# Kernel optimization log

Hardware: AMD Instinct MI355X
Metric: run time of the kernel (lower is better)

## Reference

```python
import jax, jax.numpy as jnp
import numpy as np

NUM_HEADS = 12
D_MODEL = 768
D_HEAD = D_MODEL // NUM_HEADS


def setup_inputs() -> dict:
    key = jax.random.key(0)
    k_x, k_wqkv, k_bqkv, k_wo, k_bo = jax.random.split(key, 5)
    B, S = 1, 4096
    x = jax.random.normal(k_x, (B, S, D_MODEL), dtype=jnp.float32)
    # flax Dense default init: lecun_normal for kernel, zeros for bias
    w_qkv = jax.random.normal(k_wqkv, (D_MODEL, 3 * D_MODEL), dtype=jnp.float32) / np.sqrt(D_MODEL)
    b_qkv = jnp.zeros((3 * D_MODEL,), dtype=jnp.float32)
    w_o = jax.random.normal(k_wo, (D_MODEL, D_MODEL), dtype=jnp.float32) / np.sqrt(D_MODEL)
    b_o = jnp.zeros((D_MODEL,), dtype=jnp.float32)
    return {"x": x, "w_qkv": w_qkv, "b_qkv": b_qkv, "w_o": w_o, "b_o": b_o}


def reference(x, w_qkv, b_qkv, w_o, b_o):
    B, S, _ = x.shape
    H, Dh = NUM_HEADS, D_HEAD
    qkv = jnp.einsum('bsd,de->bse', x, w_qkv) + b_qkv  # [B,S,3*D]
    q, k, v = jnp.split(qkv, 3, axis=-1)
    # [B,S,D] -> [B,H,S,Dh]
    q = q.reshape(B, S, H, Dh).transpose(0, 2, 1, 3)
    k = k.reshape(B, S, H, Dh).transpose(0, 2, 1, 3)
    v = v.reshape(B, S, H, Dh).transpose(0, 2, 1, 3)
    logits = jnp.einsum('bhqd,bhkd->bhqk', q, k) / jnp.sqrt(jnp.float32(Dh))
    weights = jax.nn.softmax(logits, axis=-1)  # deterministic=True -> no dropout
    attn = jnp.einsum('bhqk,bhkd->bhqd', weights, v)
    attn = attn.transpose(0, 2, 1, 3).reshape(B, S, H * Dh)
    return jnp.einsum('bsd,de->bse', attn, w_o) + b_o
```

## Files before the change

kernel.cpp:

```cpp
#include <hip/hip_runtime.h>

typedef unsigned short u16;
typedef __attribute__((ext_vector_type(8))) short bf16x8;
typedef __attribute__((ext_vector_type(4))) float f32x4;

#define CST 0.18033688011112042f

__device__ inline u16 f2bf(float f) {
    unsigned u;
    __builtin_memcpy(&u, &f, 4);
    unsigned r = (u + 0x7FFF + ((u >> 16) & 1)) >> 16;
    return (u16)r;
}
__device__ inline unsigned pack2(float lo, float hi) {
    return (unsigned)f2bf(lo) | ((unsigned)f2bf(hi) << 16);
}
__device__ inline unsigned fbits(float f) {
    unsigned u;
    __builtin_memcpy(&u, &f, 4);
    return u;
}
__device__ inline f32x4 fzero() {
    f32x4 z = {0.f, 0.f, 0.f, 0.f};
    return z;
}
__device__ inline f32x4 mfma16(bf16x8 a, bf16x8 b, f32x4 c) {
    return __builtin_amdgcn_mfma_f32_16x16x32_bf16(a, b, c, 0, 0, 0);
}

__device__ inline void gld_lds16(const u16* g, u16* l) {
    __builtin_amdgcn_global_load_lds(
        reinterpret_cast<const __attribute__((address_space(1))) unsigned int*>(
            reinterpret_cast<uintptr_t>(g)),
        reinterpret_cast<__attribute__((address_space(3))) unsigned int*>(
            static_cast<unsigned int>(reinterpret_cast<uintptr_t>(l))),
        16, 0, 0);
}

#define NB_WQKV (72 * 24)
#define NB_WO   (24 * 24)
#define NB_CVT  (4096 * 768 / 2048)

__global__ __launch_bounds__(256) void prep(const float* __restrict__ x,
                                            const float* __restrict__ w_qkv,
                                            const float* __restrict__ w_o,
                                            u16* __restrict__ xb,
                                            u16* __restrict__ wqkvT,
                                            u16* __restrict__ woT) {
    __shared__ float tile[32][33];
    int bid = blockIdx.x;
    int t = threadIdx.x;
    if (bid < NB_WQKV + NB_WO) {
        const float* in;
        u16* out;
        int bx, by, R, C;
        if (bid < NB_WQKV) {
            in = w_qkv; out = wqkvT; R = 768; C = 2304;
            bx = bid % 72; by = bid / 72;
        } else {
            int b2 = bid - NB_WQKV;
            in = w_o; out = woT; R = 768; C = 768;
            bx = b2 % 24; by = b2 / 24;
        }
        int c0 = bx * 32, r0 = by * 32;
        int tx = t & 31, ty = t >> 5;
#pragma unroll
        for (int j = 0; j < 32; j += 8)
            tile[ty + j][tx] = in[(size_t)(r0 + ty + j) * C + c0 + tx];
        __syncthreads();
#pragma unroll
        for (int j = 0; j < 32; j += 8)
            out[(size_t)(c0 + ty + j) * R + r0 + tx] = f2bf(tile[tx][ty + j]);
    } else {
        int i = (bid - NB_WQKV - NB_WO) * 2048 + t * 8;
        float4 a = *(const float4*)(x + i);
        float4 b = *(const float4*)(x + i + 4);
        uint4 w;
        w.x = pack2(a.x, a.y);
        w.y = pack2(a.z, a.w);
        w.z = pack2(b.x, b.y);
        w.w = pack2(b.z, b.w);
        *(uint4*)(xb + i) = w;
    }
}

__global__ __launch_bounds__(256) void vtrans(const u16* __restrict__ qkv,
                                              u16* __restrict__ vt) {
    __shared__ u16 T[64 * 136];
    int t = threadIdx.x;
    int h = blockIdx.y, kv0 = blockIdx.x * 128;
    {
        int key = t >> 1, ch = (t & 1) * 32;
        const u16* vp = qkv + (size_t)(kv0 + key) * 2304 + 1536 + h * 64 + ch;
        u16 tmp[32];
        *(uint4*)&tmp[0]  = *(const uint4*)vp;
        *(uint4*)&tmp[8]  = *(const uint4*)(vp + 8);
        *(uint4*)&tmp[16] = *(const uint4*)(vp + 16);
        *(uint4*)&tmp[24] = *(const uint4*)(vp + 24);
        int k5 = key & 31, grp = key >> 5;
        int kp = (grp << 5) | (((k5 >> 2) & 3) << 3) | ((k5 >> 4) << 2) | (k5 & 3);
#pragma unroll
        for (int j = 0; j < 32; j++) T[(ch + j) * 136 + kp] = tmp[j];
    }
    __syncthreads();
    {
        int dh = t >> 2, kc = (t & 3) * 32;
        uint4 o0 = *(const uint4*)&T[dh * 136 + kc];
        uint4 o1 = *(const uint4*)&T[dh * 136 + kc + 8];
        uint4 o2 = *(const uint4*)&T[dh * 136 + kc + 16];
        uint4 o3 = *(const uint4*)&T[dh * 136 + kc + 24];
        u16* op = vt + ((size_t)(h * 64 + dh)) * 4096 + kv0 + kc;
        *(uint4*)op = o0;
        *(uint4*)(op + 8) = o1;
        *(uint4*)(op + 16) = o2;
        *(uint4*)(op + 24) = o3;
    }
}

template <int MT, bool OUT_F32, bool SCALE_Q>
__global__ __launch_bounds__(256) void gemm_bt(const u16* __restrict__ A,
                                               const u16* __restrict__ Bt,
                                               const float* __restrict__ bias,
                                               void* __restrict__ Cv,
                                               int M, int N, int K) {
    constexpr int MI = MT / 32;
    constexpr int NA = MT / 64;
    constexpr int AH = MT * 32;
    constexpr int BH = 128 * 32;
    __shared__ u16 As[2 * AH];
    __shared__ u16 Bs[2 * BH];

    int t = threadIdx.x;
    int wave = t >> 6, lane = t & 63, quad = lane >> 4, l16 = lane & 15;
    int mbase = blockIdx.y * MT, nbase = blockIdx.x * 128;
    int mw = (wave & 1) * (MT / 2), nw = (wave >> 1) * 64;

    f32x4 acc[MI][4];
#pragma unroll
    for (int i = 0; i < MI; i++)
#pragma unroll
        for (int j = 0; j < 4; j++) acc[i][j] = fzero();

    int xqs = (lane & 3) ^ ((lane >> 3) & 3);
    const u16* AgL[NA];
    u16* AsL[NA];
#pragma unroll
    for (int j = 0; j < NA; j++) {
        int rl = wave * (MT / 4) + j * 16 + (lane >> 2);
        AgL[j] = A + (size_t)(mbase + rl) * K + xqs * 8;
        AsL[j] = As + wave * (MT / 4) * 32 + j * 512;
    }
    const u16* BgL[2];
    u16* BsL[2];
#pragma unroll
    for (int j = 0; j < 2; j++) {
        int rl = wave * 32 + j * 16 + (lane >> 2);
        BgL[j] = Bt + (size_t)(nbase + rl) * K + xqs * 8;
        BsL[j] = Bs + wave * 1024 + j * 512;
    }

    auto STAGE = [&](int buf, int kt) {
#pragma unroll
        for (int j = 0; j < NA; j++) gld_lds16(AgL[j] + kt, AsL[j] + buf * AH);
#pragma unroll
        for (int j = 0; j < 2; j++) gld_lds16(BgL[j] + kt, BsL[j] + buf * BH);
    };

    int xq = quad ^ ((l16 >> 1) & 3);
    int afo[MI], bfo[4];
#pragma unroll
    for (int i = 0; i < MI; i++) afo[i] = (mw + i * 16 + l16) * 32 + xq * 8;
#pragma unroll
    for (int i = 0; i < 4; i++) bfo[i] = (nw + i * 16 + l16) * 32 + xq * 8;

    STAGE(0, 0);
    __syncthreads();

    int cur = 0;
    for (int kt = 0; kt < K; kt += 32) {
        if (kt + 32 < K) STAGE(cur ^ 1, kt + 32);

        const u16* AsB = As + cur * AH;
        const u16* BsB = Bs + cur * BH;
        bf16x8 af[MI], bfr[4];
#pragma unroll
        for (int i = 0; i < MI; i++) af[i] = *(const bf16x8*)&AsB[afo[i]];
#pragma unroll
        for (int i = 0; i < 4; i++) bfr[i] = *(const bf16x8*)&BsB[bfo[i]];
#pragma unroll
        for (int mi = 0; mi < MI; mi++)
#pragma unroll
            for (int ni = 0; ni < 4; ni++)
                acc[mi][ni] = mfma16(af[mi], bfr[ni], acc[mi][ni]);

        __syncthreads();
        cur ^= 1;
    }

#pragma unroll
    for (int ni = 0; ni < 4; ni++) {
        int col = nbase + nw + ni * 16 + l16;
        float bv = bias[col];
        float scale = (SCALE_Q && col < 768) ? CST : 1.0f;
#pragma unroll
        for (int mi = 0; mi < MI; mi++) {
#pragma unroll
            for (int r = 0; r < 4; r++) {
                int row = mbase + mw + mi * 16 + quad * 4 + r;
                float v = (acc[mi][ni][r] + bv) * scale;
                if (OUT_F32)
                    ((float*)Cv)[(size_t)row * N + col] = v;
                else
                    ((u16*)Cv)[(size_t)row * N + col] = f2bf(v);
            }
        }
    }
}

#define SEQ 4096
#define QKV_LD 2304

__global__ __launch_bounds__(256, 4) void attn_flash(const u16* __restrict__ qkv,
                                                     const u16* __restrict__ vt,
                                                     u16* __restrict__ attn) {
    __shared__ __align__(16) char smem[32768];

    int t = threadIdx.x;
    int wave = t >> 6, lane = t & 63, quad = lane >> 4, l16 = lane & 15;
    int kw = wave & 1, qw = wave >> 1;
    int h = blockIdx.y;
    int q0 = blockIdx.x * 64;
    const int QOFF = h * 64, KOFF = 768 + h * 64;

    bf16x8 qf[2][2];
#pragma unroll
    for (int qs = 0; qs < 2; qs++) {
        const u16* qp = qkv + (size_t)(q0 + qw * 32 + qs * 16 + l16) * QKV_LD + QOFF + quad * 8;
        qf[qs][0] = *(const bf16x8*)(qp);
        qf[qs][1] = *(const bf16x8*)(qp + 32);
    }

    f32x4 o[2][4];
    float l4[2];
#pragma unroll
    for (int qs = 0; qs < 2; qs++) {
        l4[qs] = 0.f;
#pragma unroll
        for (int j = 0; j < 4; j++) o[qs][j] = fzero();
    }

    const u16* kgl[2];
    int kofs[2];
#pragma unroll
    for (int j = 0; j < 2; j++) {
        int r = wave * 16 + j * 8 + (lane >> 3);
        kgl[j] = qkv + (size_t)r * QKV_LD + KOFF +
                 (((lane & 7) ^ ((lane >> 3) & 7)) * 8);
        kofs[j] = (wave * 16 + j * 8) * 64;
    }
    const u16* vgl[2];
    int vofs[2];
#pragma unroll
    for (int j = 0; j < 2; j++) {
        int r = wave * 16 + j * 8 + (lane >> 3);
        vgl[j] = vt + (size_t)(h * 64 + r) * SEQ +
                 (((lane & 7) ^ ((lane >> 3) & 7)) * 8);
        vofs[j] = (wave * 16 + j * 8) * 64;
    }

    auto STAGE = [&](int buf, int kv) {
        u16* kb = (u16*)(smem + buf * 8192);
        u16* vb = (u16*)(smem + 16384 + buf * 8192);
#pragma unroll
        for (int j = 0; j < 2; j++) gld_lds16(kgl[j] + (size_t)kv * QKV_LD, kb + kofs[j]);
#pragma unroll
        for (int j = 0; j < 2; j++) gld_lds16(vgl[j] + kv, vb + vofs[j]);
    };

    STAGE(0, 0);
    __syncthreads();

    int cur = 0;
    int x7 = l16 & 7;
    for (int kv0 = 0; kv0 < SEQ; kv0 += 64) {
        if (kv0 + 64 < SEQ) STAGE(cur ^ 1, kv0 + 64);

        const u16* KsB = (const u16*)(smem + cur * 8192);
        const u16* VsB = (const u16*)(smem + 16384 + cur * 8192);

        bf16x8 kf[2][2];
#pragma unroll
        for (int st = 0; st < 2; st++) {
            int r = kw * 32 + st * 16 + l16;
            kf[st][0] = *(const bf16x8*)&KsB[r * 64 + (quad ^ x7) * 8];
            kf[st][1] = *(const bf16x8*)&KsB[r * 64 + ((quad + 4) ^ x7) * 8];
        }
        bf16x8 vf[4];
#pragma unroll
        for (int nt = 0; nt < 4; nt++) {
            int r = nt * 16 + l16;
            vf[nt] = *(const bf16x8*)&VsB[r * 64 + ((kw * 4 + quad) ^ x7) * 8];
        }

        __builtin_amdgcn_s_setprio(1);
#pragma unroll
        for (int qs = 0; qs < 2; qs++) {
            f32x4 s0 = mfma16(kf[0][0], qf[qs][0], fzero());
            s0 = mfma16(kf[0][1], qf[qs][1], s0);
            f32x4 s1 = mfma16(kf[1][0], qf[qs][0], fzero());
            s1 = mfma16(kf[1][1], qf[qs][1], s1);
            float p00 = exp2f(s0[0]), p01 = exp2f(s0[1]);
            float p02 = exp2f(s0[2]), p03 = exp2f(s0[3]);
            float p10 = exp2f(s1[0]), p11 = exp2f(s1[1]);
            float p12 = exp2f(s1[2]), p13 = exp2f(s1[3]);
            l4[qs] += ((p00 + p01) + (p02 + p03)) + ((p10 + p11) + (p12 + p13));
            uint4 pk;
            pk.x = __builtin_amdgcn_perm(fbits(p01), fbits(p00), 0x07060302u);
            pk.y = __builtin_amdgcn_perm(fbits(p03), fbits(p02), 0x07060302u);
            pk.z = __builtin_amdgcn_perm(fbits(p11), fbits(p10), 0x07060302u);
            pk.w = __builtin_amdgcn_perm(fbits(p13), fbits(p12), 0x07060302u);
            bf16x8 pf;
            __builtin_memcpy(&pf, &pk, 16);
#pragma unroll
            for (int nt = 0; nt < 4; nt++)
                o[qs][nt] = mfma16(pf, vf[nt], o[qs][nt]);
        }
        __builtin_amdgcn_s_setprio(0);

        __syncthreads();
        cur ^= 1;
    }

#pragma unroll
    for (int qs = 0; qs < 2; qs++) {
        l4[qs] += __shfl_xor(l4[qs], 16);
        l4[qs] += __shfl_xor(l4[qs], 32);
    }
    float* M0 = (float*)smem;
    float* Lm = (float*)(smem + 17408);
    if (lane < 16) {
        Lm[kw * 64 + qw * 32 + l16] = l4[0];
        Lm[kw * 64 + qw * 32 + 16 + l16] = l4[1];
    }
    if (kw == 1) {
#pragma unroll
        for (int nt = 0; nt < 4; nt++)
#pragma unroll
            for (int r = 0; r < 4; r++)
                M0[(qw * 32 + quad * 4 + r) * 68 + nt * 16 + l16] = o[0][nt][r];
    } else {
#pragma unroll
        for (int nt = 0; nt < 4; nt++)
#pragma unroll
            for (int r = 0; r < 4; r++)
                M0[(qw * 32 + 16 + quad * 4 + r) * 68 + nt * 16 + l16] = o[1][nt][r];
    }
    __syncthreads();
    if (kw == 0) {
#pragma unroll
        for (int r = 0; r < 4; r++) {
            int rw = qw * 32 + quad * 4 + r;
            float l = Lm[rw] + Lm[64 + rw];
            float inv = 1.0f / l;
            u16* op = attn + (size_t)(q0 + rw) * 768 + h * 64;
#pragma unroll
            for (int nt = 0; nt < 4; nt++) {
                float v = o[0][nt][r] + M0[rw * 68 + nt * 16 + l16];
                op[nt * 16 + l16] = f2bf(v * inv);
            }
        }
    } else {
#pragma unroll
        for (int r = 0; r < 4; r++) {
            int rw = qw * 32 + 16 + quad * 4 + r;
            float l = Lm[rw] + Lm[64 + rw];
            float inv = 1.0f / l;
            u16* op = attn + (size_t)(q0 + rw) * 768 + h * 64;
#pragma unroll
            for (int nt = 0; nt < 4; nt++) {
                float v = o[1][nt][r] + M0[rw * 68 + nt * 16 + l16];
                op[nt * 16 + l16] = f2bf(v * inv);
            }
        }
    }
}

extern "C" void kernel_launch(void* const* d_in, const int* in_sizes, int n_in,
                              void* d_out, int out_size, void* d_ws, size_t ws_size,
                              hipStream_t stream) {
    const float* x      = (const float*)d_in[0];
    const float* w_qkv  = (const float*)d_in[1];
    const float* b_qkv  = (const float*)d_in[2];
    const float* w_o    = (const float*)d_in[3];
    const float* b_o    = (const float*)d_in[4];
    float* out = (float*)d_out;

    u16* wqkvT = (u16*)d_ws;
    u16* woT   = wqkvT + (size_t)2304 * 768;
    u16* qkv   = woT + (size_t)768 * 768;
    u16* attnb = qkv + (size_t)4096 * 2304;
    u16* Vt    = attnb + (size_t)4096 * 768;
    u16* xb    = attnb;

    prep<<<dim3(NB_WQKV + NB_WO + NB_CVT), 256, 0, stream>>>(
        x, w_qkv, w_o, xb, wqkvT, woT);

    gemm_bt<128, false, true><<<dim3(2304 / 128, 4096 / 128), 256, 0, stream>>>(
        xb, wqkvT, b_qkv, qkv, 4096, 2304, 768);

    vtrans<<<dim3(SEQ / 128, 12), 256, 0, stream>>>(qkv, Vt);

    attn_flash<<<dim3(SEQ / 64, 12), 256, 0, stream>>>(qkv, Vt, attnb);

    gemm_bt<64, true, false><<<dim3(768 / 128, 4096 / 64), 256, 0, stream>>>(
        attnb, woT, b_o, out, 4096, 768, 768);
}
```

Before: 198.9 us.

## Split flash attention work across 8 waves with 16 query rows each

The attention kernel now launches 512 threads per block instead of 256, so each wave handles 16 query rows rather than 32. The K/V staging loads are spread over twice as many waves, and the register footprint per wave shrinks (one set of accumulators and Q fragments). This raises wave-level parallelism and latency hiding, but each wave re-reads the same K/V fragments from shared memory for half the MFMA work, which increases LDS traffic per FLOP, and the launch bounds now assume 6 blocks per CU.

New measurement: 198.8 us. No clear change (-0.0%).

```diff
diff --git a/kernel.cpp b/kernel.cpp
--- a/kernel.cpp
+++ b/kernel.cpp
@@ -220,7 +220,7 @@
 #define SEQ 4096
 #define QKV_LD 2304
 
-__global__ __launch_bounds__(256, 4) void attn_flash(const u16* __restrict__ qkv,
+__global__ __launch_bounds__(512, 6) void attn_flash(const u16* __restrict__ qkv,
                                                      const u16* __restrict__ vt,
                                                      u16* __restrict__ attn) {
     __shared__ __align__(16) char smem[32768];
@@ -232,49 +232,34 @@
     int q0 = blockIdx.x * 64;
     const int QOFF = h * 64, KOFF = 768 + h * 64;
 
-    bf16x8 qf[2][2];
-#pragma unroll
-    for (int qs = 0; qs < 2; qs++) {
-        const u16* qp = qkv + (size_t)(q0 + qw * 32 + qs * 16 + l16) * QKV_LD + QOFF + quad * 8;
-        qf[qs][0] = *(const bf16x8*)(qp);
-        qf[qs][1] = *(const bf16x8*)(qp + 32);
-    }
-
-    f32x4 o[2][4];
-    float l4[2];
-#pragma unroll
-    for (int qs = 0; qs < 2; qs++) {
-        l4[qs] = 0.f;
-#pragma unroll
-        for (int j = 0; j < 4; j++) o[qs][j] = fzero();
-    }
-
-    const u16* kgl[2];
-    int kofs[2];
-#pragma unroll
-    for (int j = 0; j < 2; j++) {
-        int r = wave * 16 + j * 8 + (lane >> 3);
-        kgl[j] = qkv + (size_t)r * QKV_LD + KOFF +
-                 (((lane & 7) ^ ((lane >> 3) & 7)) * 8);
-        kofs[j] = (wave * 16 + j * 8) * 64;
-    }
-    const u16* vgl[2];
-    int vofs[2];
-#pragma unroll
-    for (int j = 0; j < 2; j++) {
-        int r = wave * 16 + j * 8 + (lane >> 3);
-        vgl[j] = vt + (size_t)(h * 64 + r) * SEQ +
-                 (((lane & 7) ^ ((lane >> 3) & 7)) * 8);
-        vofs[j] = (wave * 16 + j * 8) * 64;
+    bf16x8 qf[2];
+    {
+        const u16* qp = qkv + (size_t)(q0 + qw * 16 + l16) * QKV_LD + QOFF + quad * 8;
+        qf[0] = *(const bf16x8*)(qp);
+        qf[1] = *(const bf16x8*)(qp + 32);
+    }
+
+    f32x4 o[4];
+    float l4 = 0.f;
+#pragma unroll
+    for (int j = 0; j < 4; j++) o[j] = fzero();
+
+    const u16* kgl;
+    const u16* vgl;
+    int sofs;
+    {
+        int r = wave * 8 + (lane >> 3);
+        int cd = (lane & 7) ^ ((lane >> 3) & 7);
+        kgl = qkv + (size_t)r * QKV_LD + KOFF + cd * 8;
+        vgl = vt + (size_t)(h * 64 + r) * SEQ + cd * 8;
+        sofs = wave * 512;
     }
 
     auto STAGE = [&](int buf, int kv) {
-        u16* kb = (u16*)(smem + buf * 8192);
-        u16* vb = (u16*)(smem + 16384 + buf * 8192);
-#pragma unroll
-        for (int j = 0; j < 2; j++) gld_lds16(kgl[j] + (size_t)kv * QKV_LD, kb + kofs[j]);
-#pragma unroll
-        for (int j = 0; j < 2; j++) gld_lds16(vgl[j] + kv, vb + vofs[j]);
+        u16* kb = (u16*)(smem + buf * 8192) + sofs;
+        u16* vb = (u16*)(smem + 16384 + buf * 8192) + sofs;
+        gld_lds16(kgl + (size_t)kv * QKV_LD, kb);
+        gld_lds16(vgl + kv, vb);
     };
 
     STAGE(0, 0);
@@ -303,17 +288,16 @@
         }
 
         __builtin_amdgcn_s_setprio(1);
-#pragma unroll
-        for (int qs = 0; qs < 2; qs++) {
-            f32x4 s0 = mfma16(kf[0][0], qf[qs][0], fzero());
-            s0 = mfma16(kf[0][1], qf[qs][1], s0);
-            f32x4 s1 = mfma16(kf[1][0], qf[qs][0], fzero());
-            s1 = mfma16(kf[1][1], qf[qs][1], s1);
+        {
+            f32x4 s0 = mfma16(kf[0][0], qf[0], fzero());
+            s0 = mfma16(kf[0][1], qf[1], s0);
+            f32x4 s1 = mfma16(kf[1][0], qf[0], fzero());
+            s1 = mfma16(kf[1][1], qf[1], s1);
             float p00 = exp2f(s0[0]), p01 = exp2f(s0[1]);
             float p02 = exp2f(s0[2]), p03 = exp2f(s0[3]);
             float p10 = exp2f(s1[0]), p11 = exp2f(s1[1]);
             float p12 = exp2f(s1[2]), p13 = exp2f(s1[3]);
-            l4[qs] += ((p00 + p01) + (p02 + p03)) + ((p10 + p11) + (p12 + p13));
+            l4 += ((p00 + p01) + (p02 + p03)) + ((p10 + p11) + (p12 + p13));
             uint4 pk;
             pk.x = __builtin_amdgcn_perm(fbits(p01), fbits(p00), 0x07060302u);
             pk.y = __builtin_amdgcn_perm(fbits(p03), fbits(p02), 0x07060302u);
@@ -323,7 +307,7 @@
             __builtin_memcpy(&pf, &pk, 16);
 #pragma unroll
             for (int nt = 0; nt < 4; nt++)
-                o[qs][nt] = mfma16(pf, vf[nt], o[qs][nt]);
+                o[nt] = mfma16(pf, vf[nt], o[nt]);
         }
         __builtin_amdgcn_s_setprio(0);
 
@@ -331,54 +315,30 @@
         cur ^= 1;
     }
 
-#pragma unroll
-    for (int qs = 0; qs < 2; qs++) {
-        l4[qs] += __shfl_xor(l4[qs], 16);
-        l4[qs] += __shfl_xor(l4[qs], 32);
-    }
+    l4 += __shfl_xor(l4, 16);
+    l4 += __shfl_xor(l4, 32);
+
     float* M0 = (float*)smem;
     float* Lm = (float*)(smem + 17408);
-    if (lane < 16) {
-        Lm[kw * 64 + qw * 32 + l16] = l4[0];
-        Lm[kw * 64 + qw * 32 + 16 + l16] = l4[1];
-    }
+    if (lane < 16) Lm[kw * 64 + qw * 16 + l16] = l4;
     if (kw == 1) {
 #pragma unroll
         for (int nt = 0; nt < 4; nt++)
 #pragma unroll
             for (int r = 0; r < 4; r++)
-                M0[(qw * 32 + quad * 4 + r) * 68 + nt * 16 + l16] = o[0][nt][r];
-    } else {
-#pragma unroll
-        for (int nt = 0; nt < 4; nt++)
-#pragma unroll
-            for (int r = 0; r < 4; r++)
-                M0[(qw * 32 + 16 + quad * 4 + r) * 68 + nt * 16 + l16] = o[1][nt][r];
+                M0[(qw * 16 + quad * 4 + r) * 68 + nt * 16 + l16] = o[nt][r];
     }
     __syncthreads();
     if (kw == 0) {
 #pragma unroll
         for (int r = 0; r < 4; r++) {
-            int rw = qw * 32 + quad * 4 + r;
-            float l = Lm[rw] + Lm[64 + rw];
-            float inv = 1.0f / l;
+            int rw = qw * 16 + quad * 4 + r;
+            float ltot = Lm[rw] + Lm[64 + rw];
+            float inv = 1.0f / ltot;
             u16* op = attn + (size_t)(q0 + rw) * 768 + h * 64;
 #pragma unroll
             for (int nt = 0; nt < 4; nt++) {
-                float v = o[0][nt][r] + M0[rw * 68 + nt * 16 + l16];
-                op[nt * 16 + l16] = f2bf(v * inv);
-            }
-        }
-    } else {
-#pragma unroll
-        for (int r = 0; r < 4; r++) {
-            int rw = qw * 32 + 16 + quad * 4 + r;
-            float l = Lm[rw] + Lm[64 + rw];
-            float inv = 1.0f / l;
-            u16* op = attn + (size_t)(q0 + rw) * 768 + h * 64;
-#pragma unroll
-            for (int nt = 0; nt < 4; nt++) {
-                float v = o[1][nt][r] + M0[rw * 68 + nt * 16 + l16];
+                float v = o[nt][r] + M0[rw * 68 + nt * 16 + l16];
                 op[nt * 16 + l16] = f2bf(v * inv);
             }
         }
@@ -410,7 +370,7 @@
 
     vtrans<<<dim3(SEQ / 128, 12), 256, 0, stream>>>(qkv, Vt);
 
-    attn_flash<<<dim3(SEQ / 64, 12), 256, 0, stream>>>(qkv, Vt, attnb);
+    attn_flash<<<dim3(SEQ / 64, 12), 512, 0, stream>>>(qkv, Vt, attnb);
 
     gemm_bt<64, true, false><<<dim3(768 / 128, 4096 / 64), 256, 0, stream>>>(
         attnb, woT, b_o, out, 4096, 768, 768);
```
